# Performance work log

Measured on AMD Instinct MI355X. Metric: run time of the kernel, lower is better.

Reference implementation:

```python
import jax, jax.numpy as jnp
import numpy as np


def setup_inputs() -> dict:
    key = jax.random.key(0)
    inputs = jax.random.normal(key, (2, 1, 256, 256, 256), dtype=jnp.float32)
    return {"inputs": inputs}


def reference(inputs) -> jnp.ndarray:
    # inputs: [B, 1, D, H, W] signed-distance-like field.
    # Equivalent to the 2x2x2 depthwise cross-correlation with kernels
    # [1,-1] along each axis, scaled by the axis size (scale = [D, H, W]),
    # followed by L2 norm over the 3 gradient channels and |norm - 1| mean.
    _, _, D, H, W = inputs.shape
    x = inputs[:, 0]  # [B, D, H, W]
    core = x[:, :-1, :-1, :-1]
    dd = (core - x[:, 1:, :-1, :-1]) * jnp.float32(D)
    dh = (core - x[:, :-1, 1:, :-1]) * jnp.float32(H)
    dw = (core - x[:, :-1, :-1, 1:]) * jnp.float32(W)
    # norm_order = 2
    norm = jnp.sqrt(dd * dd + dh * dh + dw * dw)  # [B, D-1, H-1, W-1]
    return jnp.mean(jnp.abs(norm - 1.0))
```

## Files before the change

kernel.cpp:

```cpp
#include <hip/hip_runtime.h>


#define DVOL 256
#define PLANE (DVOL * DVOL)
#define CORE 255

__device__ __forceinline__ float sq(float v) { return v * v; }

__device__ __forceinline__ float row_term(const float4 c, const float4 h1,
                                          const float4 d1, int lane, bool valid) {
    const float nx = __shfl_down(c.x, 1, 64);
    if (!valid) return 0.0f;
    float acc;
    float s;
    s = sq(c.x - d1.x) + sq(c.x - h1.x) + sq(c.x - c.y);
    acc = fabsf(fmaf(256.0f, sqrtf(s), -1.0f));
    s = sq(c.y - d1.y) + sq(c.y - h1.y) + sq(c.y - c.z);
    acc += fabsf(fmaf(256.0f, sqrtf(s), -1.0f));
    s = sq(c.z - d1.z) + sq(c.z - h1.z) + sq(c.z - c.w);
    acc += fabsf(fmaf(256.0f, sqrtf(s), -1.0f));
    if (lane != 63) {
        s = sq(c.w - d1.w) + sq(c.w - h1.w) + sq(c.w - nx);
        acc += fabsf(fmaf(256.0f, sqrtf(s), -1.0f));
    }
    return acc;
}

__global__ __launch_bounds__(256) void eik_partial(const float* __restrict__ x,
                                                   float* __restrict__ part) {
    const int tid  = threadIdx.x;
    const int lane = tid & 63;
    const int wave = tid >> 6;

    const int blk = blockIdx.x;
    const int b   = blk >> 9;
    const int dc  = (blk >> 4) & 31;
    const int hg  = (blk & 15) * 4 + wave;
    const int h   = hg * 4;
    const int d0  = dc * 8;
    const int dend = min(d0 + 8, CORE);
    const bool row3_valid = (h + 3 < CORE);
    const int ch_off = (h + 4 < DVOL) ? 4 * DVOL : 3 * DVOL;

    const float* base = x + (long long)b * (DVOL * PLANE)
                          + (long long)d0 * PLANE
                          + (long long)h * DVOL
                          + lane * 4;

    float4 r0 = *(const float4*)(base);
    float4 r1 = *(const float4*)(base + DVOL);
    float4 r2 = *(const float4*)(base + 2 * DVOL);
    float4 r3 = *(const float4*)(base + 3 * DVOL);

    float acc = 0.0f;
    for (int d = d0; d < dend; ++d) {
        const float4 cd0 = *(const float4*)(base + PLANE);
        const float4 cd1 = *(const float4*)(base + PLANE + DVOL);
        const float4 cd2 = *(const float4*)(base + PLANE + 2 * DVOL);
        const float4 cd3 = *(const float4*)(base + PLANE + 3 * DVOL);
        const float4 ch  = *(const float4*)(base + ch_off);

        acc += row_term(r0, r1, cd0, lane, true);
        acc += row_term(r1, r2, cd1, lane, true);
        acc += row_term(r2, r3, cd2, lane, true);
        acc += row_term(r3, ch, cd3, lane, row3_valid);

        r0 = cd0; r1 = cd1; r2 = cd2; r3 = cd3;
        base += PLANE;
    }

    #pragma unroll
    for (int off = 32; off > 0; off >>= 1)
        acc += __shfl_down(acc, off, 64);

    __shared__ float wsum[4];
    if (lane == 0) wsum[wave] = acc;
    __syncthreads();
    if (tid == 0)
        part[blk] = wsum[0] + wsum[1] + wsum[2] + wsum[3];
}

__global__ void eik_final(const float* __restrict__ part, float* __restrict__ out) {
    const int tid = threadIdx.x;
    double s = (double)part[tid] + (double)part[tid + 256]
             + (double)part[tid + 512] + (double)part[tid + 768];

    __shared__ double sm[256];
    sm[tid] = s;
    __syncthreads();
    #pragma unroll
    for (int off = 128; off > 0; off >>= 1) {
        if (tid < off) sm[tid] += sm[tid + off];
        __syncthreads();
    }
    if (tid == 0) {
        const double N = 2.0 * CORE * CORE * CORE;
        out[0] = (float)(sm[0] / N);
    }
}

extern "C" void kernel_launch(void* const* d_in, const int* in_sizes, int n_in,
                              void* d_out, int out_size, void* d_ws, size_t ws_size,
                              hipStream_t stream) {
    const float* x = (const float*)d_in[0];
    float* out = (float*)d_out;
    float* part = (float*)d_ws;

    eik_partial<<<1024, 256, 0, stream>>>(x, part);
    eik_final<<<1, 256, 0, stream>>>(part, out);
}
```

Measured before the change: 33.25 us.

## Fuse final reduction via last-block atomic counter and double depth chunk

Merges the two-kernel reduction into a single kernel: each block writes its partial sum, increments a global atomic counter, and the last block to finish reduces all partials and writes the mean. The depth chunk per block is doubled from 8 to 16, so the grid shrinks from 1024 to 512 blocks. This removes the second kernel launch and its dependency gap. It adds a memset launch to reset the counter, and with fewer blocks there may be less parallelism to hide memory latency.

Measured after the change: 49.75 us. 49.6% more time.

```diff
diff --git a/kernel.cpp b/kernel.cpp
--- a/kernel.cpp
+++ b/kernel.cpp
@@ -4,6 +4,8 @@
 #define DVOL 256
 #define PLANE (DVOL * DVOL)
 #define CORE 255
+#define DCH 16
+#define NBLK 512
 
 __device__ __forceinline__ float sq(float v) { return v * v; }
 
@@ -26,19 +28,21 @@
     return acc;
 }
 
-__global__ __launch_bounds__(256) void eik_partial(const float* __restrict__ x,
-                                                   float* __restrict__ part) {
+__global__ __launch_bounds__(256) void eik_fused(const float* __restrict__ x,
+                                                 float* __restrict__ part,
+                                                 unsigned int* __restrict__ counter,
+                                                 float* __restrict__ out) {
     const int tid  = threadIdx.x;
     const int lane = tid & 63;
     const int wave = tid >> 6;
 
     const int blk = blockIdx.x;
-    const int b   = blk >> 9;
-    const int dc  = (blk >> 4) & 31;
+    const int b   = blk >> 8;
+    const int dc  = (blk >> 4) & 15;
     const int hg  = (blk & 15) * 4 + wave;
     const int h   = hg * 4;
-    const int d0  = dc * 8;
-    const int dend = min(d0 + 8, CORE);
+    const int d0  = dc * DCH;
+    const int dend = min(d0 + DCH, CORE);
     const bool row3_valid = (h + 3 < CORE);
     const int ch_off = (h + 4 < DVOL) ? 4 * DVOL : 3 * DVOL;
 
@@ -74,17 +78,20 @@
         acc += __shfl_down(acc, off, 64);
 
     __shared__ float wsum[4];
+    __shared__ bool isLast;
     if (lane == 0) wsum[wave] = acc;
     __syncthreads();
-    if (tid == 0)
+    if (tid == 0) {
         part[blk] = wsum[0] + wsum[1] + wsum[2] + wsum[3];
-}
+        __threadfence();
+        unsigned int old = atomicAdd(counter, 1u);
+        isLast = (old == NBLK - 1);
+    }
+    __syncthreads();
+    if (!isLast) return;
 
-__global__ void eik_final(const float* __restrict__ part, float* __restrict__ out) {
-    const int tid = threadIdx.x;
-    double s = (double)part[tid] + (double)part[tid + 256]
-             + (double)part[tid + 512] + (double)part[tid + 768];
-
+    __threadfence();
+    double s = (double)part[tid] + (double)part[tid + 256];
     __shared__ double sm[256];
     sm[tid] = s;
     __syncthreads();
@@ -105,7 +112,8 @@
     const float* x = (const float*)d_in[0];
     float* out = (float*)d_out;
     float* part = (float*)d_ws;
+    unsigned int* counter = (unsigned int*)((char*)d_ws + 512 * sizeof(float));
 
-    eik_partial<<<1024, 256, 0, stream>>>(x, part);
-    eik_final<<<1, 256, 0, stream>>>(part, out);
+    hipMemsetAsync(counter, 0, sizeof(unsigned int), stream);
+    eik_fused<<<NBLK, 256, 0, stream>>>(x, part, counter, out);
 }
```
